# Performance work log

Hardware: AMD Instinct MI355X
Metric: run time of the kernel (lower is better)

The kernel has to match this reference:

```python
import jax, jax.numpy as jnp
import numpy as np

B, S, H, NH, HD, ROT = 4, 1024, 2048, 16, 128, 64
P = NH * HD  # attention projection size = 2048
EPS = 1e-6


def setup_inputs() -> dict:
    key = jax.random.key(0)
    ks = jax.random.split(key, 12)
    T = B * S
    # rotary frequency table [max_pos=S, 1, ROT]
    inv_freq = 1.0 / (10000.0 ** (np.arange(0, ROT, 2, dtype=np.float32) / ROT))
    f = np.outer(np.arange(S, dtype=np.float32), inv_freq)  # [S, ROT/2]
    freqs = np.concatenate([f, f], axis=-1)[:, None, :].astype(np.float32)
    sc = 0.02
    return {
        "positions": jnp.tile(jnp.arange(S, dtype=jnp.int64), B),  # per-seq positions 0..S-1
        "hidden_states": jax.random.normal(ks[0], (T, H), jnp.float32),
        "rotary_pos_emb": jnp.asarray(freqs),
        "lf1_cache": jax.random.normal(ks[1], (B, 1, H), jnp.float32) * sc,
        "lf2_cache": jax.random.normal(ks[2], (B, 1, H // 2), jnp.float32) * sc,
        "Wqk": jax.random.normal(ks[3], (2 * P, H), jnp.float32) * sc,
        "Wv": jax.random.normal(ks[4], (P, H), jnp.float32) * sc,
        "Wo": jax.random.normal(ks[5], (H, P), jnp.float32) * sc,
        "conv1_w": jax.random.normal(ks[6], (H // 2, H, 2), jnp.float32) * sc,  # [out, in, tap]
        "conv1_b": jnp.zeros((H // 2,), jnp.float32),
        "conv2_w": jax.random.normal(ks[7], (H, H // 2, 2), jnp.float32) * sc,
        "conv2_b": jnp.zeros((H,), jnp.float32),
        "ln_g": jnp.ones((H,), jnp.float32),
    }


def reference(positions, hidden_states, rotary_pos_emb, lf1_cache, lf2_cache,
              Wqk, Wv, Wo, conv1_w, conv1_b, conv2_w, conv2_b, ln_g):
    T = hidden_states.shape[0]
    scaling = HD ** -0.5

    # v projection on raw hidden states (done before lf_gate in the source)
    v = hidden_states @ Wv.T  # [T, P]

    # ---- LocalizedFiltering (two causal 2-tap convs + residual + RMSNorm),
    # vectorized over all sequences (source loops per sequence) ----
    x = hidden_states.reshape(B, S, H)
    xc = jnp.concatenate([lf1_cache, x], axis=1)  # [B, S+1, H]
    o1 = (jnp.einsum('bsh,oh->bso', xc[:, :-1], conv1_w[..., 0])
          + jnp.einsum('bsh,oh->bso', xc[:, 1:], conv1_w[..., 1]) + conv1_b)  # [B,S,H/2]
    o1c = jnp.concatenate([lf2_cache, o1], axis=1)  # [B, S+1, H/2]
    o2 = (jnp.einsum('bsc,oc->bso', o1c[:, :-1], conv2_w[..., 0])
          + jnp.einsum('bsc,oc->bso', o1c[:, 1:], conv2_w[..., 1]) + conv2_b)  # [B,S,H]
    o3 = o2 + x
    lf = o3 * jax.lax.rsqrt(jnp.mean(o3 * o3, axis=-1, keepdims=True) + EPS) * ln_g

    hs = lf.reshape(T, H)
    qk = (hs @ Wqk.T).reshape(T, NH, 2 * HD)
    q, k = jnp.split(qk, 2, axis=-1)  # each [T, NH, HD]

    # partial rotary (mscale = 1.0 since use_yarn=False)
    f = rotary_pos_emb[positions]            # [T, 1, ROT]
    cos, sin = jnp.cos(f), jnp.sin(f)

    def rope(t):
        tr, tp = t[..., :ROT], t[..., ROT:]
        t1, t2 = jnp.split(tr, 2, axis=-1)
        rot = jnp.concatenate([-t2, t1], axis=-1)
        return jnp.concatenate([tr * cos + rot * sin, tp], axis=-1)

    qb = rope(q).reshape(B, S, NH, HD)
    kb = rope(k).reshape(B, S, NH, HD)
    vb = v.reshape(B, S, NH, HD)

    # causal attention per sequence
    scores = jnp.einsum('bqhd,bkhd->bhqk', qb, kb) * scaling
    mask = jnp.tril(jnp.ones((S, S), bool))
    scores = jnp.where(mask, scores, jnp.finfo(scores.dtype).min)
    attn = jax.nn.softmax(scores, axis=-1)
    out = jnp.einsum('bhqk,bkhd->bqhd', attn, vb).reshape(T, P)
    return out @ Wo.T  # [T, H]
```

## Files before the change

### kernel.cpp

```cpp
#include <hip/hip_runtime.h>

typedef __bf16 bf16;
typedef __bf16 bf16x8 __attribute__((ext_vector_type(8)));
typedef __bf16 bf16x4 __attribute__((ext_vector_type(4)));
typedef __bf16 bf16x2 __attribute__((ext_vector_type(2)));
typedef float f32x4 __attribute__((ext_vector_type(4)));
typedef float f32x2 __attribute__((ext_vector_type(2)));

#define DEVI __device__ __forceinline__

constexpr int Bc = 4, Sc = 1024, Hc = 2048, NHc = 16, HDc = 128;
constexpr int Tc = Bc * Sc;
constexpr int Pc = NHc * HDc;
constexpr int SP = Sc + 1;

DEVI void async16(const void* g, void* l) {
  __builtin_amdgcn_global_load_lds(
      (const __attribute__((address_space(1))) unsigned int*)g,
      (__attribute__((address_space(3))) unsigned int*)l, 16, 0, 0);
}

#define BAR() __builtin_amdgcn_s_barrier()
#define LGKM0()                                          \
  do {                                                   \
    asm volatile("s_waitcnt lgkmcnt(0)" ::: "memory");   \
    __builtin_amdgcn_sched_barrier(0);                   \
  } while (0)
#define VM0() asm volatile("s_waitcnt vmcnt(0)" ::: "memory")

template <int WM, int WN, int MREP, int NREP, int EPI, int AMODE>
__global__ __launch_bounds__(512, 2) void gemm8(
    const bf16* __restrict__ A, const bf16* __restrict__ W,
    void* __restrict__ C0, void* __restrict__ C1,
    const float* __restrict__ biasf, const f32x2* __restrict__ cst,
    int M, int N, int K) {
  constexpr int BM = WM * MREP * 16;
  constexpr int BN = WN * NREP * 16;
  constexpr int MH = MREP / 2, NH = NREP / 2;
  constexpr int LA = BM / 128;
  constexpr int LB = BN / 128;
  constexpr int STG = (BM + BN) * 128;
  constexpr int OUTB = (EPI == 3) ? 4 : 2;
  constexpr int CBYTES = BM * BN * OUTB;
  constexpr int LDSB = (2 * STG > CBYTES) ? 2 * STG : CBYTES;
  __shared__ char lds[LDSB];

  const int nbx = N / BN;
  const int nwg = (M / BM) * nbx;
  int bx, by;
  if (nwg == 256 && nbx == 16) {
    const int xcd = blockIdx.x & 7, loc = blockIdx.x >> 3;
    by = (xcd >> 1) * 4 + (loc >> 3);
    bx = (xcd & 1) * 8 + (loc & 7);
  } else {
    const int wgid = (blockIdx.x & 7) * (nwg >> 3) + (blockIdx.x >> 3);
    bx = wgid % nbx;
    by = wgid / nbx;
  }
  const int m0 = by * BM, n0 = bx * BN;
  const int tid = threadIdx.x;
  const int w = tid >> 6, l = tid & 63;
  const int wm = w / WN, wn = w % WN;
  const int lr = l & 15, hi = l >> 4;

  auto vminf = [&] {
    constexpr int LL = LA + LB;
    if constexpr (LL == 4)      asm volatile("s_waitcnt vmcnt(4)" ::: "memory");
    else if constexpr (LL == 3) asm volatile("s_waitcnt vmcnt(3)" ::: "memory");
    else if constexpr (LL == 2) asm volatile("s_waitcnt vmcnt(2)" ::: "memory");
    else                        asm volatile("s_waitcnt vmcnt(0)" ::: "memory");
  };

  auto aAddr = [&](int row, int t) -> const bf16* {
    const int m = m0 + row;
    if constexpr (AMODE == 0) {
      return A + (size_t)m * K + (t << 6);
    } else if constexpr (AMODE == 1) {
      return A + (size_t)((m >> 10) * SP + (m & 1023) + 1) * K + (t << 6);
    } else {
      const int Kh2 = K >> 1, nkh = Kh2 >> 6;
      const int tap = (t >= nkh) ? 1 : 0;
      return A + (size_t)((m >> 10) * SP + (m & 1023) + tap) * Kh2 +
             ((t - (tap ? nkh : 0)) << 6);
    }
  };

  auto stageA = [&](int buf, int t, int half) {
#pragma unroll
    for (int c = 0; c < LA; ++c) {
      const int ch = c * 512 + tid;
      const int row = half * (BM / 2) + (ch >> 3);
      const int grp = ch & 7;
      async16(aAddr(row, t) + ((grp ^ (row & 7)) << 3),
              &lds[buf * STG + row * 128 + grp * 16]);
    }
  };
  auto stageB = [&](int buf, int t, int half) {
#pragma unroll
    for (int c = 0; c < LB; ++c) {
      const int ch = c * 512 + tid;
      const int row = half * (BN / 2) + (ch >> 3);
      const int grp = ch & 7;
      async16(W + (size_t)(n0 + row) * K + (t << 6) + ((grp ^ (row & 7)) << 3),
              &lds[buf * STG + BM * 128 + row * 128 + grp * 16]);
    }
  };
  auto LD = [&](const char* Lp, int row, int g) -> bf16x8 {
    return *(const bf16x8*)(Lp + ((size_t)row << 7) + ((g ^ (row & 7)) << 4));
  };

#define QUAD(MB_, NB_, FB_)                                                     \
  do {                                                                          \
    __builtin_amdgcn_s_setprio(1);                                              \
    _Pragma("unroll") for (int m = 0; m < MH; ++m)                              \
      _Pragma("unroll") for (int n = 0; n < NH; ++n)                            \
        _Pragma("unroll") for (int kk = 0; kk < 2; ++kk)                        \
          acc[(MB_) + m][(NB_) + n] = __builtin_amdgcn_mfma_f32_16x16x32_bf16(  \
              fa[m][kk], FB_[n][kk], acc[(MB_) + m][(NB_) + n], 0, 0, 0);       \
    __builtin_amdgcn_s_setprio(0);                                              \
  } while (0)

  f32x4 acc[MREP][NREP] = {};
  bf16x8 fa[MH][2], fb0[NH][2], fb1[NH][2];
  const int nk = K >> 6;

  stageA(0, 0, 0);
  stageB(0, 0, 0);
  stageA(0, 0, 1);
  stageB(0, 0, 1);
  stageA(1, 1, 0);
  stageB(1, 1, 0);
  vminf();
  BAR();

#pragma unroll 1
  for (int t = 0; t < nk; ++t) {
    const char* Lb = &lds[(t & 1) * STG];
    const int cur = t & 1, nbuf = cur ^ 1;
    const bool pf1 = (t + 1 < nk);
#pragma unroll
    for (int m = 0; m < MH; ++m) {
      const int r = wm * (MREP * 16) + m * 16 + lr;
      fa[m][0] = LD(Lb, r, hi);
      fa[m][1] = LD(Lb, r, 4 + hi);
    }
#pragma unroll
    for (int n = 0; n < NH; ++n) {
      const int r = BM + wn * (NREP * 16) + n * 16 + lr;
      fb0[n][0] = LD(Lb, r, hi);
      fb0[n][1] = LD(Lb, r, 4 + hi);
    }
    if (pf1) stageA(nbuf, t + 1, 1);
    BAR();
    LGKM0();
    QUAD(0, 0, fb0);
    BAR();
#pragma unroll
    for (int n = 0; n < NH; ++n) {
      const int r = BM + wn * (NREP * 16) + (NH + n) * 16 + lr;
      fb1[n][0] = LD(Lb, r, hi);
      fb1[n][1] = LD(Lb, r, 4 + hi);
    }
    if (pf1) stageB(nbuf, t + 1, 1);
    BAR();
    LGKM0();
    QUAD(0, NH, fb1);
    BAR();
#pragma unroll
    for (int m = 0; m < MH; ++m) {
      const int r = wm * (MREP * 16) + (MH + m) * 16 + lr;
      fa[m][0] = LD(Lb, r, hi);
      fa[m][1] = LD(Lb, r, 4 + hi);
    }
    BAR();
    LGKM0();
    QUAD(MH, NH, fb1);
    BAR();
    QUAD(MH, 0, fb0);
    if (t + 2 < nk) {
      stageA(cur, t + 2, 0);
      stageB(cur, t + 2, 0);
      vminf();
    } else {
      VM0();
    }
    BAR();
  }
#undef QUAD

  if constexpr (EPI == 0) {
    bf16* cl = (bf16*)lds;
#pragma unroll
    for (int mi = 0; mi < MREP; ++mi)
#pragma unroll
      for (int ni = 0; ni < NREP; ++ni) {
        const int col = wn * (NREP * 16) + ni * 16 + lr;
        const float bv = biasf ? biasf[n0 + col] : 0.f;
#pragma unroll
        for (int j = 0; j < 4; ++j) {
          const int row = wm * (MREP * 16) + mi * 16 + (hi << 2) + j;
          cl[row * BN + ((((col >> 3) ^ (row & 7)) << 3) | (col & 7))] =
              (bf16)(acc[mi][ni][j] + bv);
        }
      }
    __syncthreads();
    constexpr int GPR = BN / 8;
    constexpr int PT = BM * GPR / 512;
#pragma unroll
    for (int c = 0; c < PT; ++c) {
      const int ch = c * 512 + tid;
      const int row = ch / GPR, g = ch % GPR;
      bf16x8 vv = *(const bf16x8*)&cl[row * BN + ((g ^ (row & 7)) << 3)];
      *(bf16x8*)&((bf16*)C0)[(size_t)(m0 + row) * N + n0 + g * 8] = vv;
    }
  } else if constexpr (EPI == 1) {
    bf16* cl = (bf16*)lds;
#pragma unroll
    for (int mi = 0; mi < MREP; ++mi)
#pragma unroll
      for (int ni = 0; ni < NREP; ++ni) {
        const int col = wn * (NREP * 16) + ni * 16 + lr;
#pragma unroll
        for (int j = 0; j < 4; ++j) {
          const int row = wm * (MREP * 16) + mi * 16 + (hi << 2) + j;
          cl[col * BM + ((((row >> 3) ^ (col & 7)) << 3) | (row & 7))] =
              (bf16)acc[mi][ni][j];
        }
      }
    __syncthreads();
    const int s0 = m0 & 1023, bq = m0 >> 10;
    bf16* vT = (bf16*)C0;
    const size_t vbase = (((size_t)(bq * 16 + (n0 >> 7)) * 128) << 10) + s0;
    constexpr int GPR = BM / 8;
    constexpr int PT = BN * GPR / 512;
#pragma unroll
    for (int c = 0; c < PT; ++c) {
      const int ch = c * 512 + tid;
      const int d = ch / GPR, g = ch % GPR;
      bf16x8 vv = *(const bf16x8*)&cl[d * BM + ((g ^ (d & 7)) << 3)];
      *(bf16x8*)&vT[vbase + ((size_t)d << 10) + g * 8] = vv;
    }
  } else if constexpr (EPI == 2) {
    bf16* cl = (bf16*)lds;
#pragma unroll
    for (int mi = 0; mi < MREP; ++mi)
#pragma unroll
      for (int ni = 0; ni < NREP; ++ni) {
        const int col = wn * (NREP * 16) + ni * 16 + lr;
#pragma unroll
        for (int j = 0; j < 4; ++j) {
          const int row = wm * (MREP * 16) + mi * 16 + (hi << 2) + j;
          cl[row * BN + ((((col >> 3) ^ (row & 7)) << 3) | (col & 7))] =
              (bf16)acc[mi][ni][j];
        }
      }
    __syncthreads();
    const int s0 = m0 & 1023, bq = m0 >> 10, head = n0 >> 8;
    bf16* qr = (bf16*)C0;
    bf16* kr = (bf16*)C1;
    const size_t qbase = ((size_t)((bq * 16 + head) * 1024 + s0) << 7);
    constexpr int GPR = BN / 8;
    constexpr int PT = BM * GPR / 512;
#pragma unroll
    for (int c = 0; c < PT; ++c) {
      const int ch = c * 512 + tid;
      const int row = ch / GPR, g = ch % GPR;
      const int cc = g * 8;
      const int isk = cc >> 7, dd = cc & 127;
      bf16x8 vv = *(const bf16x8*)&cl[row * BN + ((g ^ (row & 7)) << 3)];
      bf16x8 out;
      if (dd < 64) {
        bf16x8 pp = *(const bf16x8*)&cl[row * BN + (((g ^ 4) ^ (row & 7)) << 3)];
        const f32x2* cp = &cst[(s0 + row) * 64 + dd];
#pragma unroll
        for (int e = 0; e < 8; ++e) {
          const f32x2 cs = cp[e];
          const float pv = (dd < 32) ? -(float)pp[e] : (float)pp[e];
          out[e] = (bf16)((float)vv[e] * cs[0] + pv * cs[1]);
        }
      } else {
        out = vv;
      }
      bf16* dst = isk ? kr : qr;
      *(bf16x8*)&dst[qbase + ((size_t)row << 7) + dd] = out;
    }
  } else {
    float* cl = (float*)lds;
#pragma unroll
    for (int mi = 0; mi < MREP; ++mi)
#pragma unroll
      for (int ni = 0; ni < NREP; ++ni) {
        const int col = wn * (NREP * 16) + ni * 16 + lr;
        const float bv = biasf ? biasf[n0 + col] : 0.f;
#pragma unroll
        for (int j = 0; j < 4; ++j) {
          const int row = wm * (MREP * 16) + mi * 16 + (hi << 2) + j;
          cl[row * BN + ((((col >> 2) ^ (row & 7)) << 2) | (col & 3))] =
              acc[mi][ni][j] + bv;
        }
      }
    __syncthreads();
    constexpr int GPR = BN / 4;
    constexpr int PT = BM * GPR / 512;
#pragma unroll
    for (int c = 0; c < PT; ++c) {
      const int ch = c * 512 + tid;
      const int row = ch / GPR, g = ch % GPR;
      f32x4 vv = *(const f32x4*)&cl[row * BN + ((g ^ (row & 7)) << 2)];
      *(f32x4*)&((float*)C0)[(size_t)(m0 + row) * N + n0 + g * 4] = vv;
    }
  }
}

template <int WM, int WN, int MREP, int NREP, int AMODE, bool OUTPAD>
__global__ __launch_bounds__(WM * WN * 64, 2) void gemm_pipe(
    const bf16* __restrict__ A, const bf16* __restrict__ W, void* __restrict__ Cout,
    const float* __restrict__ bias, int M, int N, int K) {
  constexpr int BM = WM * MREP * 16;
  constexpr int BN = WN * NREP * 16;
  constexpr int THREADS = WM * WN * 64;
  constexpr int ROWS = BM + BN;
  constexpr int CHA = BM * 4 / THREADS;
  constexpr int CHB = BN * 4 / THREADS;
  static_assert(CHA + CHB == 4, "vmcnt ledger assumes 4 loads/thread/stage");
  __shared__ bf16 lds[4][ROWS * 32];
  static_assert(BM * BN * 2 <= sizeof(lds), "C tile must fit LDS for epilogue");

  const int nbx = N / BN;
  const int nwg = (M / BM) * nbx;
  const int wgid = (blockIdx.x & 7) * (nwg >> 3) + (blockIdx.x >> 3);
  const int bx = wgid % nbx, by = wgid / nbx;
  const int m0 = by * BM, n0 = bx * BN;
  const int tid = threadIdx.x;
  const int w = tid >> 6, l = tid & 63;
  const int wm = w / WN, wn = w % WN;
  const int lr = l & 15;
  const int hi = l >> 4;

  auto aAddr = [&](int row, int t) -> const bf16* {
    const int m = m0 + row;
    if constexpr (AMODE == 2) {
      const int Kh2 = K >> 1, nkh = Kh2 >> 5;
      const int tap = (t >= nkh) ? 1 : 0;
      return A + (size_t)((m >> 10) * SP + (m & 1023) + tap) * Kh2 +
             ((t - (tap ? nkh : 0)) << 5);
    } else {
      return A + (size_t)m * K + (t << 5);
    }
  };

  auto stage = [&](int slot, int t) {
    const int k0 = t << 5;
#pragma unroll
    for (int c = 0; c < CHA; ++c) {
      const int ch = c * THREADS + tid;
      const int row = ch >> 2, cg = ch & 3;
      const int gc = (cg ^ ((row >> 1) & 3)) << 3;
      async16(aAddr(row, t) + gc, (char*)&lds[slot][0] + ch * 16);
    }
#pragma unroll
    for (int c = 0; c < CHB; ++c) {
      const int ch = c * THREADS + tid;
      const int row = ch >> 2, cg = ch & 3;
      const int gc = (cg ^ ((row >> 1) & 3)) << 3;
      async16(W + (size_t)(n0 + row) * K + k0 + gc,
              (char*)&lds[slot][0] + (BM * 4 + ch) * 16);
    }
  };

  f32x4 acc[MREP][NREP] = {};
  const int nk = K >> 5;

  stage(0, 0);
  stage(1, 1);
  stage(2, 2);
  asm volatile("s_waitcnt vmcnt(8)" ::: "memory");
  __builtin_amdgcn_s_barrier();
  __builtin_amdgcn_sched_barrier(0);

  bf16x8 fAc[MREP], fBc[NREP], fAn[MREP], fBn[NREP];
  {
    const char* nb = (const char*)&lds[0][0];
#pragma unroll
    for (int mi = 0; mi < MREP; ++mi) {
      const int r = wm * (MREP * 16) + mi * 16 + lr;
      fAc[mi] = *(const bf16x8*)(nb + r * 64 + ((hi ^ ((r >> 1) & 3)) << 4));
    }
#pragma unroll
    for (int ni = 0; ni < NREP; ++ni) {
      const int r = BM + wn * (NREP * 16) + ni * 16 + lr;
      fBc[ni] = *(const bf16x8*)(nb + r * 64 + ((hi ^ ((r >> 1) & 3)) << 4));
    }
  }

#define GSTEP(T_, CA, CB, NA, NB)                                              \
  do {                                                                         \
    if ((T_) + 2 < nk) asm volatile("s_waitcnt vmcnt(4)" ::: "memory");        \
    else               asm volatile("s_waitcnt vmcnt(0)" ::: "memory");        \
    __builtin_amdgcn_s_barrier();                                              \
    __builtin_amdgcn_sched_barrier(0);                                         \
    if ((T_) + 3 < nk) stage(((T_) + 3) & 3, (T_) + 3);                        \
    if ((T_) + 1 < nk) {                                                       \
      const char* nb = (const char*)&lds[((T_) + 1) & 3][0];                   \
      _Pragma("unroll") for (int mi = 0; mi < MREP; ++mi) {                    \
        const int r = wm * (MREP * 16) + mi * 16 + lr;                         \
        NA[mi] = *(const bf16x8*)(nb + r * 64 + ((hi ^ ((r >> 1) & 3)) << 4)); \
      }                                                                        \
      _Pragma("unroll") for (int ni = 0; ni < NREP; ++ni) {                    \
        const int r = BM + wn * (NREP * 16) + ni * 16 + lr;                    \
        NB[ni] = *(const bf16x8*)(nb + r * 64 + ((hi ^ ((r >> 1) & 3)) << 4)); \
      }                                                                        \
    }                                                                          \
    __builtin_amdgcn_s_setprio(1);                                             \
    _Pragma("unroll") for (int mi = 0; mi < MREP; ++mi)                        \
      _Pragma("unroll") for (int ni = 0; ni < NREP; ++ni)                      \
        acc[mi][ni] =                                                          \
            __builtin_amdgcn_mfma_f32_16x16x32_bf16(CA[mi], CB[ni], acc[mi][ni], 0, 0, 0); \
    __builtin_amdgcn_s_setprio(0);                                             \
  } while (0)

  for (int t = 0; t < nk; t += 2) {
    GSTEP(t, fAc, fBc, fAn, fBn);
    GSTEP(t + 1, fAn, fBn, fAc, fBc);
  }
#undef GSTEP

  __syncthreads();
  {
    bf16* cl = (bf16*)&lds[0][0];
#pragma unroll
    for (int mi = 0; mi < MREP; ++mi) {
#pragma unroll
      for (int ni = 0; ni < NREP; ++ni) {
        const int col = wn * (NREP * 16) + ni * 16 + lr;
        const float bv = bias ? bias[n0 + col] : 0.f;
#pragma unroll
        for (int j = 0; j < 4; ++j) {
          const int row = wm * (MREP * 16) + mi * 16 + (hi << 2) + j;
          cl[row * BN + ((((col >> 3) ^ (row & 7)) << 3) | (col & 7))] =
              (bf16)(acc[mi][ni][j] + bv);
        }
      }
    }
    __syncthreads();
    constexpr int GPR = BN / 8;
    constexpr int PT = BM * GPR / THREADS;
#pragma unroll
    for (int c = 0; c < PT; ++c) {
      const int ch = c * THREADS + tid;
      const int row = ch / GPR, g = ch % GPR;
      const int mr = m0 + row;
      const size_t orow = OUTPAD ? (size_t)((mr >> 10) * SP + (mr & 1023) + 1)
                                 : (size_t)mr;
      bf16x8 vv = *(const bf16x8*)&cl[row * BN + ((g ^ (row & 7)) << 3)];
      *(bf16x8*)&((bf16*)Cout)[orow * N + n0 + g * 8] = vv;
    }
  }
}

__global__ void k_f2b4(const float* __restrict__ in, bf16* __restrict__ out, int n4) {
  int i = blockIdx.x * 256 + threadIdx.x;
  if (i >= n4) return;
  float4 v = ((const float4*)in)[i];
  bf16x4 o = {(bf16)v.x, (bf16)v.y, (bf16)v.z, (bf16)v.w};
  ((bf16x4*)out)[i] = o;
}

__global__ void k_deint(const float* __restrict__ in, bf16* __restrict__ out,
                        int O, int Hd) {
  int i = blockIdx.x * 256 + threadIdx.x;
  if (i >= O * (Hd >> 1)) return;
  int o = i / (Hd >> 1), h0 = (i % (Hd >> 1)) * 2;
  float4 v = *(const float4*)&in[(size_t)o * Hd * 2 + h0 * 2];
  bf16x2 t0 = {(bf16)v.x, (bf16)v.z};
  bf16x2 t1 = {(bf16)v.y, (bf16)v.w};
  *(bf16x2*)&out[(size_t)o * 2 * Hd + h0] = t0;
  *(bf16x2*)&out[(size_t)o * 2 * Hd + Hd + h0] = t1;
}

__global__ void k_trig(const float* __restrict__ rot, f32x2* __restrict__ cst) {
  int i = blockIdx.x * 256 + threadIdx.x;
  float f = rot[i];
  f32x2 cs = {cosf(f), sinf(f)};
  cst[i] = cs;
}

__global__ void k_build_hsbp(const float* __restrict__ hid, const float* __restrict__ lf1,
                             const float* __restrict__ lf2,
                             bf16* __restrict__ hsbp, bf16* __restrict__ o1p) {
  int idx = blockIdx.x * 256 + threadIdx.x;
  int t = idx >> 11, h = idx & 2047;
  int b = t >> 10, s = t & 1023;
  hsbp[((size_t)(b * SP + s + 1) << 11) + h] = (bf16)hid[idx];
  if (idx < Bc * Hc) {
    int bb = idx >> 11, hh = idx & 2047;
    hsbp[((size_t)(bb * SP) << 11) + hh] = (bf16)lf1[idx];
  }
  if (idx < Bc * 1024) {
    int bb = idx >> 10, cc = idx & 1023;
    o1p[((size_t)(bb * SP) << 10) + cc] = (bf16)lf2[idx];
  }
}

__global__ __launch_bounds__(256) void k_rmsnorm(const bf16* __restrict__ o2,
                                                 const float* __restrict__ hid,
                                                 const float* __restrict__ g,
                                                 bf16* __restrict__ lf) {
  int t = blockIdx.x, tid = threadIdx.x;
  size_t base = ((size_t)t << 11) + tid * 8;
  bf16x8 ov = *(const bf16x8*)&o2[base];
  const float* hp = &hid[base];
  float vals[8];
  float ss = 0.f;
#pragma unroll
  for (int i = 0; i < 8; ++i) {
    float x = (float)ov[i] + hp[i];
    vals[i] = x;
    ss += x * x;
  }
#pragma unroll
  for (int off = 1; off < 64; off <<= 1) ss += __shfl_xor(ss, off);
  __shared__ float red[4];
  if ((tid & 63) == 0) red[tid >> 6] = ss;
  __syncthreads();
  float tot = red[0] + red[1] + red[2] + red[3];
  float inv = rsqrtf(tot * (1.f / 2048.f) + 1e-6f);
  bf16x8 o;
#pragma unroll
  for (int i = 0; i < 8; ++i) o[i] = (bf16)(vals[i] * inv * g[tid * 8 + i]);
  *(bf16x8*)&lf[base] = o;
}

__global__ __launch_bounds__(256, 2) void k_attn(const bf16* __restrict__ qr,
                                                 const bf16* __restrict__ kr,
                                                 const bf16* __restrict__ vT,
                                                 bf16* __restrict__ att) {
  __shared__ bf16 Ks[2][64 * 128];
  __shared__ bf16 Vs[2][128 * 64];
  __shared__ bf16 plds[4][16 * 64];
  const int bid = blockIdx.x;
  const int xcd = bid & 7, jj = bid >> 3;
  const int bn = xcd * 8 + (jj >> 3);
  const int pr = jj & 7;
  const int tid = threadIdx.x, w = tid >> 6, l = tid & 63;
  const int lr = l & 15, hi = l >> 4;
  const bf16* kb = kr + ((size_t)bn << 17);
  const bf16* vb = vT + ((size_t)bn << 17);
  const int b = bn >> 4, hh = bn & 15;
  const float scaling = 0.08838834764831845f;

  auto stage = [&](int buf, int kt) {
#pragma unroll
    for (int c = 0; c < 4; ++c) {
      int chunk = c * 256 + tid;
      int prow = chunk >> 4, pcg = chunk & 15;
      async16(kb + ((size_t)(kt * 64 + prow) << 7) + ((pcg ^ (prow & 7)) << 3),
              (char*)&Ks[buf][0] + chunk * 16);
    }
#pragma unroll
    for (int c = 0; c < 4; ++c) {
      int chunk = c * 256 + tid;
      int prow = chunk >> 3, pcg = chunk & 7;
      async16(vb + ((size_t)prow << 10) + kt * 64 + ((pcg ^ (prow & 7)) << 3),
              (char*)&Vs[buf][0] + chunk * 16);
    }
  };

#pragma unroll 1
  for (int phase = 0; phase < 2; ++phase) {
    const int qt = phase ? (15 - pr) : pr;
    const int qg0 = qt * 64 + w * 16;
    const bf16* qb = qr + ((size_t)(bn * 1024 + qg0) << 7);
    bf16x8 qf[4];
#pragma unroll
    for (int ks = 0; ks < 4; ++ks) qf[ks] = *(const bf16x8*)&qb[lr * 128 + ks * 32 + hi * 8];
    f32x4 oacc[8] = {};
    float mrow[4] = {-1e30f, -1e30f, -1e30f, -1e30f};
    float lrow[4] = {0.f, 0.f, 0.f, 0.f};
    const int nkb = qt + 1;

    stage(0, 0);
    __syncthreads();

    for (int kbt = 0; kbt < nkb; ++kbt) {
      const int cur = kbt & 1;
      if (kbt + 1 < nkb) stage(cur ^ 1, kbt + 1);

      f32x4 sacc[4] = {};
#pragma unroll
      for (int n = 0; n < 4; ++n) {
        const int krow = n * 16 + lr;
#pragma unroll
        for (int ks = 0; ks < 4; ++ks) {
          bf16x8 kf = *(const bf16x8*)&Ks[cur][(krow << 7) + ((((ks << 2) | hi) ^ (krow & 7)) << 3)];
          sacc[n] = __builtin_amdgcn_mfma_f32_16x16x32_bf16(qf[ks], kf, sacc[n], 0, 0, 0);
        }
      }
      const bool needmask = (kbt * 64 + 63 > qg0);
#pragma unroll
      for (int n = 0; n < 4; ++n) {
        int kg = kbt * 64 + n * 16 + lr;
#pragma unroll
        for (int j = 0; j < 4; ++j) {
          float sv = sacc[n][j] * scaling;
          if (needmask && kg > qg0 + hi * 4 + j) sv = -1e30f;
          sacc[n][j] = sv;
        }
      }
      float sf[4];
#pragma unroll
      for (int j = 0; j < 4; ++j) {
        float pm = fmaxf(fmaxf(sacc[0][j], sacc[1][j]), fmaxf(sacc[2][j], sacc[3][j]));
        pm = fmaxf(pm, __shfl_xor(pm, 1));
        pm = fmaxf(pm, __shfl_xor(pm, 2));
        pm = fmaxf(pm, __shfl_xor(pm, 4));
        pm = fmaxf(pm, __shfl_xor(pm, 8));
        float mn = fmaxf(mrow[j], pm);
        sf[j] = __expf(mrow[j] - mn);
        mrow[j] = mn;
      }
#pragma unroll
      for (int n = 0; n < 4; ++n)
#pragma unroll
        for (int j = 0; j < 4; ++j) sacc[n][j] = __expf(sacc[n][j] - mrow[j]);
#pragma unroll
      for (int j = 0; j < 4; ++j) {
        float ps = sacc[0][j] + sacc[1][j] + sacc[2][j] + sacc[3][j];
        ps += __shfl_xor(ps, 1);
        ps += __shfl_xor(ps, 2);
        ps += __shfl_xor(ps, 4);
        ps += __shfl_xor(ps, 8);
        lrow[j] = lrow[j] * sf[j] + ps;
      }
#pragma unroll
      for (int dt = 0; dt < 8; ++dt)
#pragma unroll
        for (int j = 0; j < 4; ++j) oacc[dt][j] *= sf[j];
#pragma unroll
      for (int n = 0; n < 4; ++n)
#pragma unroll
        for (int j = 0; j < 4; ++j)
          plds[w][(hi * 4 + j) * 64 + n * 16 + lr] = (bf16)sacc[n][j];
      asm volatile("s_waitcnt lgkmcnt(0)" ::: "memory");
#pragma unroll
      for (int ks2 = 0; ks2 < 2; ++ks2) {
        bf16x8 pf = *(const bf16x8*)&plds[w][lr * 64 + ks2 * 32 + hi * 8];
#pragma unroll
        for (int dt = 0; dt < 8; ++dt) {
          const int vrow = dt * 16 + lr;
          bf16x8 vf = *(const bf16x8*)&Vs[cur][(vrow << 6) + ((((ks2 << 2) | hi) ^ (lr & 7)) << 3)];
          oacc[dt] = __builtin_amdgcn_mfma_f32_16x16x32_bf16(pf, vf, oacc[dt], 0, 0, 0);
        }
      }
      __syncthreads();
    }

#pragma unroll
    for (int j = 0; j < 4; ++j) {
      float inv = 1.f / lrow[j];
      int qg = qg0 + hi * 4 + j;
      size_t obase = ((size_t)(b * 1024 + qg) << 11) + hh * 128;
#pragma unroll
      for (int dt = 0; dt < 8; ++dt) att[obase + dt * 16 + lr] = (bf16)(oacc[dt][j] * inv);
    }
  }
}

extern "C" void kernel_launch(void* const* d_in, const int* in_sizes, int n_in,
                              void* d_out, int out_size, void* d_ws, size_t ws_size,
                              hipStream_t stream) {
  const float* hid = (const float*)d_in[1];
  const float* rot = (const float*)d_in[2];
  const float* lf1 = (const float*)d_in[3];
  const float* lf2 = (const float*)d_in[4];
  const float* Wqk = (const float*)d_in[5];
  const float* Wv  = (const float*)d_in[6];
  const float* Wo  = (const float*)d_in[7];
  const float* c1w = (const float*)d_in[8];
  const float* c1b = (const float*)d_in[9];
  const float* c2w = (const float*)d_in[10];
  const float* c2b = (const float*)d_in[11];
  const float* lng = (const float*)d_in[12];
  float* outp = (float*)d_out;
  char* ws = (char*)d_ws;

  const size_t MB = 1ull << 20;
  bf16* Wslot = (bf16*)(ws + 0 * MB);
  bf16* hsbp  = (bf16*)(ws + 16 * MB);
  bf16* att   = (bf16*)(ws + 16 * MB);
  bf16* o1p   = (bf16*)(ws + 34 * MB);
  bf16* o2    = (bf16*)(ws + 43 * MB);
  bf16* lfb   = (bf16*)(ws + 59 * MB);
  bf16* vT    = (bf16*)(ws + 75 * MB);
  bf16* qr    = (bf16*)(ws + 91 * MB);
  bf16* kr    = (bf16*)(ws + 107 * MB);
  f32x2* cst  = (f32x2*)(ws + 123 * MB);

  auto f2b = [&](const float* in, bf16* out, int n) {
    int n4 = n / 4;
    k_f2b4<<<(n4 + 255) / 256, 256, 0, stream>>>(in, out, n4);
  };

  k_trig<<<Sc * 64 / 256, 256, 0, stream>>>(rot, cst);
  k_build_hsbp<<<Tc * Hc / 256, 256, 0, stream>>>(hid, lf1, lf2, hsbp, o1p);

  f2b(Wv, Wslot, 2048 * 2048);
  gemm8<4, 2, 4, 4, 1, 1><<<256, 512, 0, stream>>>(hsbp, Wslot, vT, nullptr, nullptr,
                                                   nullptr, Tc, Pc, Hc);

  k_deint<<<(1024 * 1024 + 255) / 256, 256, 0, stream>>>(c1w, Wslot, 1024, 2048);
  gemm_pipe<2, 2, 4, 4, 2, true><<<256, 256, 0, stream>>>(hsbp, Wslot, o1p, c1b,
                                                          Tc, 1024, 4096);

  k_deint<<<(2048 * 512 + 255) / 256, 256, 0, stream>>>(c2w, Wslot, 2048, 1024);
  gemm8<4, 2, 4, 4, 0, 2><<<256, 512, 0, stream>>>(o1p, Wslot, o2, nullptr, c2b,
                                                   nullptr, Tc, 2048, 2048);

  k_rmsnorm<<<Tc, 256, 0, stream>>>(o2, hid, lng, lfb);

  f2b(Wqk, Wslot, 4096 * 2048);
  gemm8<2, 4, 8, 4, 2, 0><<<256, 512, 0, stream>>>(lfb, Wslot, qr, kr, nullptr, cst,
                                                   Tc, 4096, Hc);

  k_attn<<<Bc * NHc * 8, 256, 0, stream>>>(qr, kr, vT, att);

  f2b(Wo, Wslot, 2048 * 2048);
  gemm8<4, 2, 4, 4, 3, 0><<<256, 512, 0, stream>>>(att, Wslot, outp, nullptr, nullptr,
                                                   nullptr, Tc, 2048, 2048);
}
```

Measured before the change: 346.8 us.

## Use lazy softmax rescaling in attention, raise MFMA priority, fuse trig kernel

The attention loop now rescales the output accumulator and running max only when some lane's block max exceeds the stored max by a threshold (FA4-style lazy rescale), skipping the exp and accumulator multiply on most iterations. MFMA sections are wrapped in s_setprio to favour matrix-issue waves. The cos/sin table computation is folded into the hidden-state build kernel, removing one launch. Lazy rescaling lets unnormalised exponentials grow up to e^8, which slightly risks bf16 precision of P.

```diff
diff --git a/kernel.cpp b/kernel.cpp
--- a/kernel.cpp
+++ b/kernel.cpp
@@ -478,16 +478,10 @@
   *(bf16x2*)&out[(size_t)o * 2 * Hd + Hd + h0] = t1;
 }
 
-__global__ void k_trig(const float* __restrict__ rot, f32x2* __restrict__ cst) {
-  int i = blockIdx.x * 256 + threadIdx.x;
-  float f = rot[i];
-  f32x2 cs = {cosf(f), sinf(f)};
-  cst[i] = cs;
-}
-
 __global__ void k_build_hsbp(const float* __restrict__ hid, const float* __restrict__ lf1,
-                             const float* __restrict__ lf2,
-                             bf16* __restrict__ hsbp, bf16* __restrict__ o1p) {
+                             const float* __restrict__ lf2, const float* __restrict__ rot,
+                             bf16* __restrict__ hsbp, bf16* __restrict__ o1p,
+                             f32x2* __restrict__ cst) {
   int idx = blockIdx.x * 256 + threadIdx.x;
   int t = idx >> 11, h = idx & 2047;
   int b = t >> 10, s = t & 1023;
@@ -499,6 +493,11 @@
   if (idx < Bc * 1024) {
     int bb = idx >> 10, cc = idx & 1023;
     o1p[((size_t)(bb * SP) << 10) + cc] = (bf16)lf2[idx];
+  }
+  if (idx < Sc * 64) {
+    float f = rot[idx];
+    f32x2 cs = {cosf(f), sinf(f)};
+    cst[idx] = cs;
   }
 }
 
@@ -548,6 +547,7 @@
   const bf16* vb = vT + ((size_t)bn << 17);
   const int b = bn >> 4, hh = bn & 15;
   const float scaling = 0.08838834764831845f;
+  const float THR = 8.f;
 
   auto stage = [&](int buf, int kt) {
 #pragma unroll
@@ -587,6 +587,7 @@
       if (kbt + 1 < nkb) stage(cur ^ 1, kbt + 1);
 
       f32x4 sacc[4] = {};
+      __builtin_amdgcn_s_setprio(1);
 #pragma unroll
       for (int n = 0; n < 4; ++n) {
         const int krow = n * 16 + lr;
@@ -596,6 +597,7 @@
           sacc[n] = __builtin_amdgcn_mfma_f32_16x16x32_bf16(qf[ks], kf, sacc[n], 0, 0, 0);
         }
       }
+      __builtin_amdgcn_s_setprio(0);
       const bool needmask = (kbt * 64 + 63 > qg0);
 #pragma unroll
       for (int n = 0; n < 4; ++n) {
@@ -607,17 +609,30 @@
           sacc[n][j] = sv;
         }
       }
-      float sf[4];
+      float pm[4];
 #pragma unroll
       for (int j = 0; j < 4; ++j) {
-        float pm = fmaxf(fmaxf(sacc[0][j], sacc[1][j]), fmaxf(sacc[2][j], sacc[3][j]));
-        pm = fmaxf(pm, __shfl_xor(pm, 1));
-        pm = fmaxf(pm, __shfl_xor(pm, 2));
-        pm = fmaxf(pm, __shfl_xor(pm, 4));
-        pm = fmaxf(pm, __shfl_xor(pm, 8));
-        float mn = fmaxf(mrow[j], pm);
-        sf[j] = __expf(mrow[j] - mn);
-        mrow[j] = mn;
+        float p = fmaxf(fmaxf(sacc[0][j], sacc[1][j]), fmaxf(sacc[2][j], sacc[3][j]));
+        p = fmaxf(p, __shfl_xor(p, 1));
+        p = fmaxf(p, __shfl_xor(p, 2));
+        p = fmaxf(p, __shfl_xor(p, 4));
+        p = fmaxf(p, __shfl_xor(p, 8));
+        pm[j] = p;
+      }
+      float sf[4] = {1.f, 1.f, 1.f, 1.f};
+      bool needup = (pm[0] > mrow[0] + THR) || (pm[1] > mrow[1] + THR) ||
+                    (pm[2] > mrow[2] + THR) || (pm[3] > mrow[3] + THR);
+      if (__any(needup)) {
+#pragma unroll
+        for (int j = 0; j < 4; ++j) {
+          float mn = fmaxf(mrow[j], pm[j]);
+          sf[j] = __expf(mrow[j] - mn);
+          mrow[j] = mn;
+        }
+#pragma unroll
+        for (int dt = 0; dt < 8; ++dt)
+#pragma unroll
+          for (int j = 0; j < 4; ++j) oacc[dt][j] *= sf[j];
       }
 #pragma unroll
       for (int n = 0; n < 4; ++n)
@@ -633,15 +648,12 @@
         lrow[j] = lrow[j] * sf[j] + ps;
       }
 #pragma unroll
-      for (int dt = 0; dt < 8; ++dt)
-#pragma unroll
-        for (int j = 0; j < 4; ++j) oacc[dt][j] *= sf[j];
-#pragma unroll
       for (int n = 0; n < 4; ++n)
 #pragma unroll
         for (int j = 0; j < 4; ++j)
           plds[w][(hi * 4 + j) * 64 + n * 16 + lr] = (bf16)sacc[n][j];
       asm volatile("s_waitcnt lgkmcnt(0)" ::: "memory");
+      __builtin_amdgcn_s_setprio(1);
 #pragma unroll
       for (int ks2 = 0; ks2 < 2; ++ks2) {
         bf16x8 pf = *(const bf16x8*)&plds[w][lr * 64 + ks2 * 32 + hi * 8];
@@ -652,6 +664,7 @@
           oacc[dt] = __builtin_amdgcn_mfma_f32_16x16x32_bf16(pf, vf, oacc[dt], 0, 0, 0);
         }
       }
+      __builtin_amdgcn_s_setprio(0);
       __syncthreads();
     }
 
@@ -701,8 +714,7 @@
     k_f2b4<<<(n4 + 255) / 256, 256, 0, stream>>>(in, out, n4);
   };
 
-  k_trig<<<Sc * 64 / 256, 256, 0, stream>>>(rot, cst);
-  k_build_hsbp<<<Tc * Hc / 256, 256, 0, stream>>>(hid, lf1, lf2, hsbp, o1p);
+  k_build_hsbp<<<Tc * Hc / 256, 256, 0, stream>>>(hid, lf1, lf2, rot, hsbp, o1p, cst);
 
   f2b(Wv, Wslot, 2048 * 2048);
   gemm8<4, 2, 4, 4, 1, 1><<<256, 512, 0, stream>>>(hsbp, Wslot, vT, nullptr, nullptr,
```

Measured after the change: 346.4 us. No clear change (-0.1%).
